# Kernel tuning notes

Measured on AMD Instinct MI355X. Metric: run time of the kernel, lower is better.

The kernel has to match this reference:

```python
import jax, jax.numpy as jnp
import numpy as np

BATCH, SEQ, D_IN, D_OUT = 32, 1024, 128, 128
NEG_SLOPE = 0.1


def setup_inputs() -> dict:
    key = jax.random.key(0)
    k1, k2, k3, k4 = jax.random.split(key, 4)
    nodes = jax.random.normal(k1, (BATCH, SEQ, D_IN), dtype=jnp.float32)
    adjacent = jax.random.randint(k2, (BATCH, SEQ, SEQ), 0, 2, dtype=jnp.int32)
    W = jax.random.normal(k3, (D_IN, D_OUT), dtype=jnp.float32) / np.sqrt(D_IN)
    B = jax.random.normal(k4, (D_IN, D_OUT), dtype=jnp.float32) / np.sqrt(D_IN)
    return {"nodes": nodes, "adjacent": adjacent, "W": W, "B": B}


def reference(nodes, adjacent, W, B):
    # mask[b, out, in] = 1 if edge (out -> in) present
    mask = (adjacent != 0).astype(nodes.dtype)
    # counts[b, in] = in-degree (number of 'out' neighbors pooled per target node)
    counts = mask.sum(axis=1)                               # [b, s_in]
    # segment-sum of neighbor features: pooled[b, in, d] = sum_out mask * nodes[b, out, d]
    pooled = jnp.einsum('boi,bod->bid', mask, nodes)        # [b, s_in, d]
    # mean over neighbors; nodes with zero degree get no pooled contribution
    pooled = jnp.where(counts[..., None] > 0,
                       pooled / jnp.maximum(counts, 1.0)[..., None],
                       jnp.zeros((), dtype=nodes.dtype))
    updated = nodes @ B + pooled @ W                        # [b, s, d_out]
    return jax.nn.leaky_relu(updated, negative_slope=NEG_SLOPE)
```

## Files before the change

kernel.cpp:

```cpp
#include <hip/hip_runtime.h>
#include <hip/hip_bf16.h>

#define SEQ 1024
#define DIM 128
#define NEG_SLOPE 0.1f

typedef __bf16 bf16x8 __attribute__((ext_vector_type(8)));
typedef float f32x4v __attribute__((ext_vector_type(4)));

union LdsU {
    struct {
        unsigned short mask_t[64][72];
        unsigned short nodes_t[128][72];
    } s;
    unsigned short pooled[64][136];
};

__device__ __forceinline__ unsigned short bfb(float f) {
    __bf16 h = (__bf16)f;
    return __builtin_bit_cast(unsigned short, h);
}
__device__ __forceinline__ unsigned mpack(int x0, int x1) {
    unsigned m0 = (x0 != 0) ? 0x3F80u : 0u;
    unsigned m1 = (x1 != 0) ? 0x3F80u : 0u;
    return m0 | (m1 << 16);
}

__global__ __launch_bounds__(256, 2)
void gcn_fused(const float* __restrict__ nodes,
               const int* __restrict__ adj,
               const float* __restrict__ W,
               const float* __restrict__ Bm,
               float* __restrict__ out)
{
    __shared__ LdsU u;

    const int bid   = blockIdx.x;
    const int xcd   = bid & 7;
    const int slot  = bid >> 3;
    const int batch = ((slot >> 4) << 3) | xcd;
    const int mtile = slot & 15;
    const int i0    = mtile << 6;

    const int tid  = threadIdx.x;
    const int wave = tid >> 6;
    const int lane = tid & 63;
    const int wm   = wave >> 1;
    const int wn   = wave & 1;
    const int lrow = lane & 15;
    const int quad = lane >> 4;

    const int*   __restrict__ adj_b   = adj   + (size_t)batch * SEQ * SEQ;
    const float* __restrict__ nodes_b = nodes + (size_t)batch * SEQ * DIM;

    const int a_row = (tid >> 4) * 4;
    const int a_col = (tid & 15) * 4;
    const int n_row = (tid >> 5) * 4;
    const int n_col = (tid & 31) * 4;

    f32x4v acc[2][4] = {};
    f32x4v acc_cnt[2] = {};

    bf16x8 ones;
    #pragma unroll
    for (int j = 0; j < 8; ++j) ones[j] = __builtin_bit_cast(__bf16, (unsigned short)0x3F80);

    int4   A[4];
    float4 N[8];

    auto load_chunk = [&](int o0) {
        const int* pa = adj_b + (size_t)(o0 + a_row) * SEQ + (i0 + a_col);
        #pragma unroll
        for (int r = 0; r < 4; ++r) A[r] = *(const int4*)(pa + (size_t)r * SEQ);
        const float* pn = nodes_b + (size_t)(o0 + n_row) * DIM + n_col;
        #pragma unroll
        for (int it = 0; it < 2; ++it)
            #pragma unroll
            for (int r = 0; r < 4; ++r)
                N[it * 4 + r] = *(const float4*)(pn + (size_t)(it * 32 + r) * DIM);
    };

    load_chunk(0);

    for (int chunk = 0; chunk < 16; ++chunk) {
        __syncthreads();
        #pragma unroll
        for (int j = 0; j < 4; ++j) {
            uint2 w;
            w.x = mpack(((const int*)&A[0])[j], ((const int*)&A[1])[j]);
            w.y = mpack(((const int*)&A[2])[j], ((const int*)&A[3])[j]);
            *(uint2*)&u.s.mask_t[a_col + j][a_row] = w;
        }
        #pragma unroll
        for (int it = 0; it < 2; ++it) {
            #pragma unroll
            for (int j = 0; j < 4; ++j) {
                uint2 w;
                w.x = (unsigned)bfb(((const float*)&N[it*4+0])[j]) |
                      ((unsigned)bfb(((const float*)&N[it*4+1])[j]) << 16);
                w.y = (unsigned)bfb(((const float*)&N[it*4+2])[j]) |
                      ((unsigned)bfb(((const float*)&N[it*4+3])[j]) << 16);
                *(uint2*)&u.s.nodes_t[n_col + j][it * 32 + n_row] = w;
            }
        }
        __syncthreads();
        if (chunk < 15) load_chunk((chunk + 1) * 64);

        #pragma unroll
        for (int kk = 0; kk < 2; ++kk) {
            bf16x8 av[2], bv[4];
            av[0] = *(const bf16x8*)&u.s.mask_t[wm * 32 + lrow][kk * 32 + quad * 8];
            av[1] = *(const bf16x8*)&u.s.mask_t[wm * 32 + 16 + lrow][kk * 32 + quad * 8];
            #pragma unroll
            for (int nf = 0; nf < 4; ++nf)
                bv[nf] = *(const bf16x8*)&u.s.nodes_t[wn * 64 + nf * 16 + lrow][kk * 32 + quad * 8];
            #pragma unroll
            for (int mf = 0; mf < 2; ++mf) {
                #pragma unroll
                for (int nf = 0; nf < 4; ++nf)
                    acc[mf][nf] = __builtin_amdgcn_mfma_f32_16x16x32_bf16(av[mf], bv[nf], acc[mf][nf], 0, 0, 0);
                acc_cnt[mf] = __builtin_amdgcn_mfma_f32_16x16x32_bf16(av[mf], ones, acc_cnt[mf], 0, 0, 0);
            }
        }
    }

    __syncthreads();
    #pragma unroll
    for (int mf = 0; mf < 2; ++mf) {
        #pragma unroll
        for (int r = 0; r < 4; ++r) {
            const int row = wm * 32 + mf * 16 + quad * 4 + r;
            const float cnt = acc_cnt[mf][r];
            const float inv = (cnt > 0.5f) ? 1.0f / cnt : 0.0f;
            #pragma unroll
            for (int nf = 0; nf < 4; ++nf) {
                const int col = wn * 64 + nf * 16 + lrow;
                u.pooled[row][col] = bfb(acc[mf][nf][r] * inv);
            }
        }
    }
    __syncthreads();

    f32x4v acc2[2][4] = {};
    const int d_b0 = wn * 64 + lrow;

    #pragma unroll
    for (int ks = 0; ks < 4; ++ks) {
        const int k0 = ks * 32 + quad * 8;
        bf16x8 av[2];
        #pragma unroll
        for (int mf = 0; mf < 2; ++mf)
            av[mf] = *(const bf16x8*)&u.pooled[wm * 32 + mf * 16 + lrow][k0];
        bf16x8 bv[4];
        const float* pw = W + (size_t)k0 * DIM + d_b0;
        #pragma unroll
        for (int nf = 0; nf < 4; ++nf) {
            #pragma unroll
            for (int j = 0; j < 8; ++j)
                bv[nf][j] = (__bf16)pw[j * DIM + nf * 16];
        }
        #pragma unroll
        for (int mf = 0; mf < 2; ++mf)
            #pragma unroll
            for (int nf = 0; nf < 4; ++nf)
                acc2[mf][nf] = __builtin_amdgcn_mfma_f32_16x16x32_bf16(av[mf], bv[nf], acc2[mf][nf], 0, 0, 0);
    }

    #pragma unroll
    for (int ks = 0; ks < 4; ++ks) {
        const int k0 = ks * 32 + quad * 8;
        bf16x8 av[2];
        #pragma unroll
        for (int mf = 0; mf < 2; ++mf) {
            const float* p = nodes_b + (size_t)(i0 + wm * 32 + mf * 16 + lrow) * DIM + k0;
            const float4 f1 = *(const float4*)p;
            const float4 f2 = *(const float4*)(p + 4);
            av[mf][0] = (__bf16)f1.x; av[mf][1] = (__bf16)f1.y;
            av[mf][2] = (__bf16)f1.z; av[mf][3] = (__bf16)f1.w;
            av[mf][4] = (__bf16)f2.x; av[mf][5] = (__bf16)f2.y;
            av[mf][6] = (__bf16)f2.z; av[mf][7] = (__bf16)f2.w;
        }
        bf16x8 bv[4];
        const float* pB = Bm + (size_t)k0 * DIM + d_b0;
        #pragma unroll
        for (int nf = 0; nf < 4; ++nf) {
            #pragma unroll
            for (int j = 0; j < 8; ++j)
                bv[nf][j] = (__bf16)pB[j * DIM + nf * 16];
        }
        #pragma unroll
        for (int mf = 0; mf < 2; ++mf)
            #pragma unroll
            for (int nf = 0; nf < 4; ++nf)
                acc2[mf][nf] = __builtin_amdgcn_mfma_f32_16x16x32_bf16(av[mf], bv[nf], acc2[mf][nf], 0, 0, 0);
    }

    float* out_b = out + (size_t)batch * SEQ * DIM;
    #pragma unroll
    for (int mf = 0; mf < 2; ++mf) {
        #pragma unroll
        for (int nf = 0; nf < 4; ++nf) {
            const int col = wn * 64 + nf * 16 + lrow;
            #pragma unroll
            for (int r = 0; r < 4; ++r) {
                const int row = i0 + wm * 32 + mf * 16 + quad * 4 + r;
                const float x = acc2[mf][nf][r];
                out_b[(size_t)row * DIM + col] = (x > 0.0f) ? x : NEG_SLOPE * x;
            }
        }
    }
}

extern "C" void kernel_launch(void* const* d_in, const int* in_sizes, int n_in,
                              void* d_out, int out_size, void* d_ws, size_t ws_size,
                              hipStream_t stream) {
    const float* nodes = (const float*)d_in[0];
    const int*   adj   = (const int*)d_in[1];
    const float* W     = (const float*)d_in[2];
    const float* Bm    = (const float*)d_in[3];
    float*       out   = (float*)d_out;
    gcn_fused<<<dim3(512), dim3(256), 0, stream>>>(nodes, adj, W, Bm, out);
}
```

Baseline: 225.4 us.

## Double-buffer LDS with two-deep register prefetch and XOR-swizzled layout

Replaces the single padded LDS tile with two XOR-swizzled buffers and two register staging sets, so global loads run two chunks ahead and each iteration needs one barrier instead of two. The swizzle replaces row padding to avoid bank conflicts on the 128-bit MFMA operand reads. A custom barrier waits only on LDS counters. This doubles LDS use (48 KB) and raises register pressure, which may lower occupancy under launch_bounds(256,2).

```diff
diff --git a/kernel.cpp b/kernel.cpp
--- a/kernel.cpp
+++ b/kernel.cpp
@@ -8,13 +8,20 @@
 typedef __bf16 bf16x8 __attribute__((ext_vector_type(8)));
 typedef float f32x4v __attribute__((ext_vector_type(4)));
 
-union LdsU {
-    struct {
-        unsigned short mask_t[64][72];
-        unsigned short nodes_t[128][72];
-    } s;
-    unsigned short pooled[64][136];
-};
+#define BUF_STRIDE 24576
+#define NODES_OFF  8192
+
+__device__ __forceinline__ int swz(int row, int unit) {
+    const int x  = row >> 2;
+    const int fx = ((x & 3) | ((x & 1) << 2)) ^ ((x >> 2) & 7);
+    return row * 128 + ((unit ^ fx) << 4);
+}
+
+__device__ __forceinline__ void bar() {
+    asm volatile("s_waitcnt lgkmcnt(0)" ::: "memory");
+    __builtin_amdgcn_s_barrier();
+    __builtin_amdgcn_sched_barrier(0);
+}
 
 __device__ __forceinline__ unsigned short bfb(float f) {
     __bf16 h = (__bf16)f;
@@ -33,7 +40,7 @@
                const float* __restrict__ Bm,
                float* __restrict__ out)
 {
-    __shared__ LdsU u;
+    __shared__ alignas(16) unsigned char lds[2 * BUF_STRIDE];
 
     const int bid   = blockIdx.x;
     const int xcd   = bid & 7;
@@ -58,6 +65,11 @@
     const int n_row = (tid >> 5) * 4;
     const int n_col = (tid & 31) * 4;
 
+    const int m_unit = (tid >> 4) >> 1;
+    const int m_sub  = ((tid >> 4) & 1) * 8;
+    const int n_unit = (tid >> 5) >> 1;
+    const int n_sub  = ((tid >> 5) & 1) * 8;
+
     f32x4v acc[2][4] = {};
     f32x4v acc_cnt[2] = {};
 
@@ -65,10 +77,10 @@
     #pragma unroll
     for (int j = 0; j < 8; ++j) ones[j] = __builtin_bit_cast(__bf16, (unsigned short)0x3F80);
 
-    int4   A[4];
-    float4 N[8];
-
-    auto load_chunk = [&](int o0) {
+    int4   A0[4], A1[4];
+    float4 N0[8], N1[8];
+
+    auto load_chunk = [&](int o0, int4 (&A)[4], float4 (&N)[8]) {
         const int* pa = adj_b + (size_t)(o0 + a_row) * SEQ + (i0 + a_col);
         #pragma unroll
         for (int r = 0; r < 4; ++r) A[r] = *(const int4*)(pa + (size_t)r * SEQ);
@@ -80,16 +92,15 @@
                 N[it * 4 + r] = *(const float4*)(pn + (size_t)(it * 32 + r) * DIM);
     };
 
-    load_chunk(0);
-
-    for (int chunk = 0; chunk < 16; ++chunk) {
-        __syncthreads();
+    auto write_lds = [&](int base, const int4 (&A)[4], const float4 (&N)[8]) {
+        unsigned char* mb = lds + base;
+        unsigned char* nb = lds + base + NODES_OFF;
         #pragma unroll
         for (int j = 0; j < 4; ++j) {
             uint2 w;
             w.x = mpack(((const int*)&A[0])[j], ((const int*)&A[1])[j]);
             w.y = mpack(((const int*)&A[2])[j], ((const int*)&A[3])[j]);
-            *(uint2*)&u.s.mask_t[a_col + j][a_row] = w;
+            *(uint2*)(mb + swz(a_col + j, m_unit) + m_sub) = w;
         }
         #pragma unroll
         for (int it = 0; it < 2; ++it) {
@@ -100,20 +111,22 @@
                       ((unsigned)bfb(((const float*)&N[it*4+1])[j]) << 16);
                 w.y = (unsigned)bfb(((const float*)&N[it*4+2])[j]) |
                       ((unsigned)bfb(((const float*)&N[it*4+3])[j]) << 16);
-                *(uint2*)&u.s.nodes_t[n_col + j][it * 32 + n_row] = w;
-            }
-        }
-        __syncthreads();
-        if (chunk < 15) load_chunk((chunk + 1) * 64);
-
+                *(uint2*)(nb + swz(n_col + j, 4 * it + n_unit) + n_sub) = w;
+            }
+        }
+    };
+
+    auto compute = [&](int base) {
+        const unsigned char* mb = lds + base;
+        const unsigned char* nb = lds + base + NODES_OFF;
         #pragma unroll
         for (int kk = 0; kk < 2; ++kk) {
             bf16x8 av[2], bv[4];
-            av[0] = *(const bf16x8*)&u.s.mask_t[wm * 32 + lrow][kk * 32 + quad * 8];
-            av[1] = *(const bf16x8*)&u.s.mask_t[wm * 32 + 16 + lrow][kk * 32 + quad * 8];
+            av[0] = *(const bf16x8*)(mb + swz(wm * 32 +      lrow, 4 * kk + quad));
+            av[1] = *(const bf16x8*)(mb + swz(wm * 32 + 16 + lrow, 4 * kk + quad));
             #pragma unroll
             for (int nf = 0; nf < 4; ++nf)
-                bv[nf] = *(const bf16x8*)&u.s.nodes_t[wn * 64 + nf * 16 + lrow][kk * 32 + quad * 8];
+                bv[nf] = *(const bf16x8*)(nb + swz(wn * 64 + nf * 16 + lrow, 4 * kk + quad));
             #pragma unroll
             for (int mf = 0; mf < 2; ++mf) {
                 #pragma unroll
@@ -122,9 +135,27 @@
                 acc_cnt[mf] = __builtin_amdgcn_mfma_f32_16x16x32_bf16(av[mf], ones, acc_cnt[mf], 0, 0, 0);
             }
         }
-    }
-
-    __syncthreads();
+    };
+
+    load_chunk(0,   A0, N0);
+    load_chunk(64,  A1, N1);
+    write_lds(0, A0, N0);
+    load_chunk(128, A0, N0);
+    bar();
+
+    for (int cc = 0; cc < 8; ++cc) {
+        const int c0 = cc * 2;
+        compute(0);
+        write_lds(BUF_STRIDE, A1, N1);
+        if (c0 + 3 < 16) load_chunk((c0 + 3) * 64, A1, N1);
+        bar();
+        compute(BUF_STRIDE);
+        if (c0 + 2 < 16) write_lds(0, A0, N0);
+        if (c0 + 4 < 16) load_chunk((c0 + 4) * 64, A0, N0);
+        bar();
+    }
+
+    unsigned short (*pooled)[136] = (unsigned short (*)[136])(void*)lds;
     #pragma unroll
     for (int mf = 0; mf < 2; ++mf) {
         #pragma unroll
@@ -135,7 +166,7 @@
             #pragma unroll
             for (int nf = 0; nf < 4; ++nf) {
                 const int col = wn * 64 + nf * 16 + lrow;
-                u.pooled[row][col] = bfb(acc[mf][nf][r] * inv);
+                pooled[row][col] = bfb(acc[mf][nf][r] * inv);
             }
         }
     }
@@ -150,7 +181,7 @@
         bf16x8 av[2];
         #pragma unroll
         for (int mf = 0; mf < 2; ++mf)
-            av[mf] = *(const bf16x8*)&u.pooled[wm * 32 + mf * 16 + lrow][k0];
+            av[mf] = *(const bf16x8*)&pooled[wm * 32 + mf * 16 + lrow][k0];
         bf16x8 bv[4];
         const float* pw = W + (size_t)k0 * DIM + d_b0;
         #pragma unroll
```

New measurement: 222.6 us. About the same (-1.3%).
